# Kernel optimization log

Hardware: AMD Instinct MI355X
Metric: run time of the kernel (lower is better)

## Reference

```python
import jax, jax.numpy as jnp
import numpy as np

B, L, D_IN = 4, 2048, 1024
D_KEY, D_VAL = 1024, 1024
N_SLOTS, TOPK = 32768, 16
TEMP = 0.1
EPS = 1e-5


def layer_norm(x, g, b):
    mu = jnp.mean(x, axis=-1, keepdims=True)
    var = jnp.var(x, axis=-1, keepdims=True)
    return (x - mu) * jax.lax.rsqrt(var + EPS) * g + b


def setup_inputs() -> dict:
    key = jax.random.key(0)
    ks = jax.random.split(key, 8)
    s_in = 1.0 / np.sqrt(D_IN)
    s_ft = 1.0 / np.sqrt(D_IN + D_VAL + 1)
    return {
        "h_in": jax.random.normal(ks[0], (B, L, D_IN), jnp.float32),
        "Wk": jax.random.normal(ks[1], (D_IN, D_KEY), jnp.float32) * s_in,
        "bk": jnp.zeros((D_KEY,), jnp.float32),
        "cube_keys": jax.random.normal(ks[2], (N_SLOTS, D_KEY), jnp.float32),
        "cube_vals": jax.random.normal(ks[3], (N_SLOTS, D_VAL), jnp.float32) * 0.1,
        "ln_in_g": jnp.ones((D_IN,), jnp.float32),
        "ln_in_b": jnp.zeros((D_IN,), jnp.float32),
        "ln_pred_g": jnp.ones((D_VAL,), jnp.float32),
        "ln_pred_b": jnp.zeros((D_VAL,), jnp.float32),
        "W1": jax.random.normal(ks[4], (D_IN + D_VAL + 1, D_IN), jnp.float32) * s_ft,
        "b1": jnp.zeros((D_IN,), jnp.float32),
        "W2": jax.random.normal(ks[5], (D_IN, 1), jnp.float32) * s_in,
        "b2": jnp.zeros((1,), jnp.float32),
    }


def reference(h_in, Wk, bk, cube_keys, cube_vals, ln_in_g, ln_in_b,
              ln_pred_g, ln_pred_b, W1, b1, W2, b2):
    Bv, Lv, Dv = h_in.shape
    # key projection -> [B*L, d_key]
    keys = (jnp.einsum('bld,dk->blk', h_in, Wk) + bk).reshape(Bv * Lv, -1)
    # cube kNN query: cosine similarity against slot keys
    kn = keys * jax.lax.rsqrt(jnp.sum(keys * keys, -1, keepdims=True) + 1e-8)
    mn = cube_keys * jax.lax.rsqrt(jnp.sum(cube_keys * cube_keys, -1, keepdims=True) + 1e-8)
    sims = kn @ mn.T                                   # [BL, N]
    top_sims, idx = jax.lax.top_k(sims, TOPK)          # [BL, K]
    w = jax.nn.softmax(top_sims / TEMP, axis=-1)       # retrieval weights
    vals = jnp.take(cube_vals, idx, axis=0)            # [BL, K, d_val] gather
    pred = jnp.einsum('nk,nkd->nd', w, vals).reshape(Bv, Lv, -1)
    conf = ((top_sims[:, 0] + 1.0) * 0.5).reshape(Bv, Lv, 1)
    # gate
    feats = jnp.concatenate([layer_norm(h_in, ln_in_g, ln_in_b),
                             layer_norm(pred, ln_pred_g, ln_pred_b),
                             conf], axis=-1)
    hmid = jax.nn.silu(jnp.einsum('blf,fd->bld', feats, W1) + b1)
    alpha = jnp.clip(jax.nn.sigmoid(jnp.einsum('bld,do->blo', hmid, W2) + b2), 0.0, 1.0)
    # blend (y_teacher is None): (1-a)*h + a*(h+pred)
    y_out = (1.0 - alpha) * h_in + alpha * (h_in + pred)
    return y_out, jnp.mean(alpha), jnp.mean(conf)
```

## Files before the change

### kernel.cpp

```cpp
#include <hip/hip_runtime.h>
#include <hip/hip_bf16.h>
#include <cstdint>
#include <cstddef>

typedef __bf16 bf16;
typedef __bf16 bf16x4 __attribute__((ext_vector_type(4)));
typedef __bf16 bf16x8 __attribute__((ext_vector_type(8)));
typedef float  f32x4  __attribute__((ext_vector_type(4)));

#define BL      8192
#define DDIM    1024
#define NSLOTS  32768
#define NSPLIT  8
#define SLOTS_PER (NSLOTS / NSPLIT)

#define WS_MN    ((size_t)0)
#define WS_PRED  ((size_t)0)
#define WS_HBF   ((size_t)67108864)
#define WS_HMID  WS_HBF
#define WS_WKT   ((size_t)83886080)
#define WS_W1T   ((size_t)85983232)
#define WS_KEYS  ((size_t)90177536)
#define WS_FEATS WS_KEYS
#define WS_KN    ((size_t)123731968)
#define WS_TPK   ((size_t)140509184)
#define WS_CONF  ((size_t)148897792)

__device__ __forceinline__ void async16(const void* g, void* l) {
  __builtin_amdgcn_global_load_lds(
      (const __attribute__((address_space(1))) void*)g,
      (__attribute__((address_space(3))) void*)(uintptr_t)(uint32_t)(uintptr_t)l,
      16, 0, 0);
}

__device__ __forceinline__ void stage_tile(const bf16* __restrict__ src, int ld,
                                           bf16* lds, int tid) {
  const int wave = tid >> 6;
#pragma unroll
  for (int issue = 0; issue < 2; ++issue) {
    const int gi  = issue * 256 + tid;
    const int row = gi >> 2;
    const int gc  = gi & 3;
    const bf16* g = src + (size_t)row * ld + gc * 8;
    bf16* l = lds + (size_t)(issue * 256 + wave * 64) * 8;
    async16(g, l);
  }
}

__device__ __forceinline__ f32x4 mfma_bf16(bf16x8 a, bf16x8 b, f32x4 c) {
  return __builtin_amdgcn_mfma_f32_16x16x32_bf16(a, b, c, 0, 0, 0);
}

__device__ __forceinline__ float block_sum(float v, float* red) {
#pragma unroll
  for (int off = 32; off > 0; off >>= 1) v += __shfl_xor(v, off, 64);
  const int tid = threadIdx.x;
  if ((tid & 63) == 0) red[tid >> 6] = v;
  __syncthreads();
  v = red[0] + red[1] + red[2] + red[3];
  __syncthreads();
  return v;
}

__global__ void cvt_bf16_kernel(const float* __restrict__ in, bf16* __restrict__ out, int n4) {
  int i = blockIdx.x * blockDim.x + threadIdx.x;
  if (i >= n4) return;
  f32x4 v = *(const f32x4*)(in + (size_t)i * 4);
  bf16x4 o = {(bf16)v.x, (bf16)v.y, (bf16)v.z, (bf16)v.w};
  *(bf16x4*)(out + (size_t)i * 4) = o;
}

__global__ void transpose_f32_bf16(const float* __restrict__ in, bf16* __restrict__ out,
                                   int R, int C) {
  __shared__ float tile[32][33];
  const int c0 = blockIdx.x * 32, r0 = blockIdx.y * 32;
  for (int i = threadIdx.y; i < 32; i += 8)
    tile[i][threadIdx.x] = in[(size_t)(r0 + i) * C + c0 + threadIdx.x];
  __syncthreads();
  for (int i = threadIdx.y; i < 32; i += 8)
    out[(size_t)(c0 + i) * R + r0 + threadIdx.x] = (bf16)tile[threadIdx.x][i];
}

__global__ __launch_bounds__(256) void rownorm_kernel(const float* __restrict__ in,
                                                      bf16* __restrict__ out) {
  __shared__ float red[4];
  const int row = blockIdx.x, t = threadIdx.x;
  f32x4 v = *(const f32x4*)(in + (size_t)row * 1024 + t * 4);
  float sq = v.x * v.x + v.y * v.y + v.z * v.z + v.w * v.w;
  sq = block_sum(sq, red);
  float sc = rsqrtf(sq + 1e-8f);
  bf16x4 o = {(bf16)(v.x * sc), (bf16)(v.y * sc), (bf16)(v.z * sc), (bf16)(v.w * sc)};
  *(bf16x4*)(out + (size_t)row * 1024 + t * 4) = o;
}

template <int EPI>
__global__ __launch_bounds__(256, 2) void gemm_bt_kernel(
    const bf16* __restrict__ A, const bf16* __restrict__ Bm, int Kd,
    float* __restrict__ Cf, bf16* __restrict__ Cb,
    const float* __restrict__ bias, const float* __restrict__ conf,
    const float* __restrict__ w1c) {
  __shared__ bf16 As[128 * 32];
  __shared__ bf16 Bs[128 * 32];
  const int tid = threadIdx.x;
  const int lane = tid & 63, wave = tid >> 6;
  const int wr = (wave >> 1) * 64, wc = (wave & 1) * 64;
  const int m0 = blockIdx.x * 128, n0 = blockIdx.y * 128;
  const int ar = lane & 15, ak = (lane >> 4) * 8;

  f32x4 acc[4][4];
#pragma unroll
  for (int i = 0; i < 4; ++i)
#pragma unroll
    for (int j = 0; j < 4; ++j) acc[i][j] = (f32x4){0.f, 0.f, 0.f, 0.f};

  for (int k0 = 0; k0 < Kd; k0 += 32) {
    __syncthreads();
    stage_tile(A + (size_t)m0 * Kd + k0, Kd, As, tid);
    stage_tile(Bm + (size_t)n0 * Kd + k0, Kd, Bs, tid);
    __syncthreads();
    bf16x8 af[4], bfr[4];
#pragma unroll
    for (int i = 0; i < 4; ++i)
      af[i] = *(const bf16x8*)(As + (wr + i * 16 + ar) * 32 + ak);
#pragma unroll
    for (int j = 0; j < 4; ++j)
      bfr[j] = *(const bf16x8*)(Bs + (wc + j * 16 + ar) * 32 + ak);
#pragma unroll
    for (int i = 0; i < 4; ++i)
#pragma unroll
      for (int j = 0; j < 4; ++j)
        acc[i][j] = mfma_bf16(af[i], bfr[j], acc[i][j]);
  }

  const int mq = (lane >> 4) * 4, nq = lane & 15;
#pragma unroll
  for (int i = 0; i < 4; ++i)
#pragma unroll
    for (int j = 0; j < 4; ++j)
#pragma unroll
      for (int r = 0; r < 4; ++r) {
        const int m = m0 + wr + i * 16 + mq + r;
        const int n = n0 + wc + j * 16 + nq;
        float x = acc[i][j][r];
        if (EPI == 0) {
          Cf[(size_t)m * 1024 + n] = x + bias[n];
        } else {
          x += bias[n] + conf[m] * w1c[n];
          x = x / (1.f + expf(-x));
          Cb[(size_t)m * 1024 + n] = (bf16)x;
        }
      }
}


__device__ __forceinline__ void scan64(const float* __restrict__ cs_row, int base_slot,
                                       uint32_t (&tk)[16], float& thrF) {
#pragma unroll
  for (int g = 0; g < 16; ++g) {
    f32x4 v4 = *(const f32x4*)(cs_row + g * 4);
#pragma unroll
    for (int e = 0; e < 4; ++e) {
      const float v = v4[e];
      if (v > thrF) {
        const uint32_t u = __float_as_uint(v);
        uint32_t cur = ((u ^ 0x80000000u) & 0xFFFF8000u) | (uint32_t)(base_slot + g * 4 + e);
#pragma unroll
        for (int p = 0; p < 16; ++p) {
          const uint32_t old = tk[p];
          const uint32_t mx = old > cur ? old : cur;
          const uint32_t mn_ = old > cur ? cur : old;
          tk[p] = mx;
          cur = mn_;
        }
        thrF = __uint_as_float((tk[15] & 0xFFFF8000u) ^ 0x80000000u);
      }
    }
  }
}

__global__ __launch_bounds__(256, 2) void sims_topk_kernel(
    const bf16* __restrict__ kn, const bf16* __restrict__ mn,
    uint32_t* __restrict__ tpk) {
  __shared__ bf16 As[128 * 32];
  __shared__ bf16 Bs0[128 * 32];
  __shared__ bf16 Bs1[128 * 32];
  __shared__ float Cs[64 * 132];

  const int tid = threadIdx.x;
  const int lane = tid & 63, wave = tid >> 6;
  const int wr = (wave >> 1) * 64, wc = (wave & 1) * 64;
  const int split = blockIdx.x;
  const int m0 = blockIdx.y * 128;
  const int sbeg = split * SLOTS_PER;
  const int ar = lane & 15, ak = (lane >> 4) * 8;
  const int mq = (lane >> 4) * 4, nq = lane & 15;

  const int rowloc = tid & 63;
  const int half = tid >> 7;
  const bool scanA = ((tid & 127) < 64);

  uint32_t tk[16];
#pragma unroll
  for (int j = 0; j < 16; ++j) tk[j] = 0u;
  float thrF = __uint_as_float(0x80000000u);

  for (int it = 0; it < SLOTS_PER / 256; ++it) {
    f32x4 acc[2][4][4];
#pragma unroll
    for (int c = 0; c < 2; ++c)
#pragma unroll
      for (int i = 0; i < 4; ++i)
#pragma unroll
        for (int j = 0; j < 4; ++j) acc[c][i][j] = (f32x4){0.f, 0.f, 0.f, 0.f};

    const int n0 = sbeg + it * 256;
    for (int k0 = 0; k0 < 1024; k0 += 32) {
      __syncthreads();
      stage_tile(kn + (size_t)m0 * 1024 + k0, 1024, As, tid);
      stage_tile(mn + (size_t)n0 * 1024 + k0, 1024, Bs0, tid);
      stage_tile(mn + (size_t)(n0 + 128) * 1024 + k0, 1024, Bs1, tid);
      __syncthreads();
      bf16x8 af[4], b0[4], b1[4];
#pragma unroll
      for (int i = 0; i < 4; ++i)
        af[i] = *(const bf16x8*)(As + (wr + i * 16 + ar) * 32 + ak);
#pragma unroll
      for (int j = 0; j < 4; ++j) {
        b0[j] = *(const bf16x8*)(Bs0 + (wc + j * 16 + ar) * 32 + ak);
        b1[j] = *(const bf16x8*)(Bs1 + (wc + j * 16 + ar) * 32 + ak);
      }
#pragma unroll
      for (int i = 0; i < 4; ++i)
#pragma unroll
        for (int j = 0; j < 4; ++j) {
          acc[0][i][j] = mfma_bf16(af[i], b0[j], acc[0][i][j]);
          acc[1][i][j] = mfma_bf16(af[i], b1[j], acc[1][i][j]);
        }
    }

#pragma unroll
    for (int cc = 0; cc < 2; ++cc) {
      const int slot_base = n0 + cc * 128 + half * 64;
      __syncthreads();
      if (wave < 2) {
#pragma unroll
        for (int i = 0; i < 4; ++i)
#pragma unroll
          for (int j = 0; j < 4; ++j)
#pragma unroll
            for (int r = 0; r < 4; ++r)
              Cs[(i * 16 + mq + r) * 132 + wc + j * 16 + nq] = acc[cc][i][j][r];
      }
      __syncthreads();
      if (scanA) scan64(&Cs[rowloc * 132 + half * 64], slot_base, tk, thrF);
      __syncthreads();
      if (wave >= 2) {
#pragma unroll
        for (int i = 0; i < 4; ++i)
#pragma unroll
          for (int j = 0; j < 4; ++j)
#pragma unroll
            for (int r = 0; r < 4; ++r)
              Cs[(i * 16 + mq + r) * 132 + wc + j * 16 + nq] = acc[cc][i][j][r];
      }
      __syncthreads();
      if (!scanA) scan64(&Cs[rowloc * 132 + half * 64], slot_base, tk, thrF);
    }
  }

  const int row = m0 + (tid & 127);
  uint32_t* dst = tpk + (((size_t)row * NSPLIT + split) * 2 + half) * 16;
#pragma unroll
  for (int j = 0; j < 16; ++j) dst[j] = tk[j];
}

__global__ __launch_bounds__(256) void merge_pred_kernel(
    const uint32_t* __restrict__ tpk, const float* __restrict__ vals,
    float* __restrict__ pred, float* __restrict__ conf) {
  __shared__ uint32_t ks[256];
  __shared__ float sv[16];
  __shared__ int si[16];
  __shared__ float sw[16];
  const int row = blockIdx.x, t = threadIdx.x;
  const uint32_t k = tpk[(size_t)row * 256 + t];
  ks[t] = k;
  __syncthreads();
  int rank = 0;
  for (int j = 0; j < 256; ++j) rank += (ks[j] > k);
  if (rank < 16) {
    sv[rank] = __uint_as_float((k & 0xFFFF8000u) ^ 0x80000000u);
    si[rank] = (int)(k & 0x7FFFu);
  }
  __syncthreads();
  if (t == 0) {
    const float m = sv[0];
    float s = 0.f;
#pragma unroll
    for (int q = 0; q < 16; ++q) {
      float e = expf((sv[q] - m) * 10.f);
      sw[q] = e;
      s += e;
    }
    const float inv = 1.f / s;
#pragma unroll
    for (int q = 0; q < 16; ++q) sw[q] *= inv;
    conf[row] = (m + 1.f) * 0.5f;
  }
  __syncthreads();
  const int col = t * 4;
  f32x4 a = (f32x4){0.f, 0.f, 0.f, 0.f};
#pragma unroll
  for (int q = 0; q < 16; ++q) {
    f32x4 vv = *(const f32x4*)(vals + (size_t)si[q] * 1024 + col);
    a += vv * sw[q];
  }
  *(f32x4*)(pred + (size_t)row * 1024 + col) = a;
}

__global__ __launch_bounds__(256) void feats_kernel(
    const float* __restrict__ h, const float* __restrict__ pred,
    const float* __restrict__ gin, const float* __restrict__ bin,
    const float* __restrict__ gpr, const float* __restrict__ bpr,
    bf16* __restrict__ feats) {
  __shared__ float red[4];
  const int row = blockIdx.x, t = threadIdx.x;
  {
    f32x4 v = *(const f32x4*)(h + (size_t)row * 1024 + t * 4);
    float s = v.x + v.y + v.z + v.w;
    float sq = v.x * v.x + v.y * v.y + v.z * v.z + v.w * v.w;
    s = block_sum(s, red);
    sq = block_sum(sq, red);
    const float mean = s * (1.f / 1024.f);
    const float rstd = rsqrtf(sq * (1.f / 1024.f) - mean * mean + 1e-5f);
    f32x4 g = *(const f32x4*)(gin + t * 4);
    f32x4 b = *(const f32x4*)(bin + t * 4);
    bf16x4 o = {(bf16)((v.x - mean) * rstd * g.x + b.x),
                (bf16)((v.y - mean) * rstd * g.y + b.y),
                (bf16)((v.z - mean) * rstd * g.z + b.z),
                (bf16)((v.w - mean) * rstd * g.w + b.w)};
    *(bf16x4*)(feats + (size_t)row * 2048 + t * 4) = o;
  }
  {
    f32x4 v = *(const f32x4*)(pred + (size_t)row * 1024 + t * 4);
    float s = v.x + v.y + v.z + v.w;
    float sq = v.x * v.x + v.y * v.y + v.z * v.z + v.w * v.w;
    s = block_sum(s, red);
    sq = block_sum(sq, red);
    const float mean = s * (1.f / 1024.f);
    const float rstd = rsqrtf(sq * (1.f / 1024.f) - mean * mean + 1e-5f);
    f32x4 g = *(const f32x4*)(gpr + t * 4);
    f32x4 b = *(const f32x4*)(bpr + t * 4);
    bf16x4 o = {(bf16)((v.x - mean) * rstd * g.x + b.x),
                (bf16)((v.y - mean) * rstd * g.y + b.y),
                (bf16)((v.z - mean) * rstd * g.z + b.z),
                (bf16)((v.w - mean) * rstd * g.w + b.w)};
    *(bf16x4*)(feats + (size_t)row * 2048 + 1024 + t * 4) = o;
  }
}

__global__ __launch_bounds__(256) void final_kernel(
    const bf16* __restrict__ hmid, const float* __restrict__ W2,
    const float* __restrict__ b2, const float* __restrict__ h,
    const float* __restrict__ pred, const float* __restrict__ conf,
    float* __restrict__ out) {
  __shared__ float red[4];
  const int row = blockIdx.x, t = threadIdx.x;
  float s = 0.f;
#pragma unroll
  for (int j = 0; j < 4; ++j) {
    const int c = t + 256 * j;
    s += (float)hmid[(size_t)row * 1024 + c] * W2[c];
  }
  s = block_sum(s, red);
  float alpha = 1.f / (1.f + expf(-(s + b2[0])));
  alpha = fminf(fmaxf(alpha, 0.f), 1.f);
  f32x4 hv = *(const f32x4*)(h + (size_t)row * 1024 + t * 4);
  f32x4 pv = *(const f32x4*)(pred + (size_t)row * 1024 + t * 4);
  f32x4 y = hv + pv * alpha;
  *(f32x4*)(out + (size_t)row * 1024 + t * 4) = y;
  if (t == 0) {
    atomicAdd(out + 8388608, alpha * (1.f / 8192.f));
    atomicAdd(out + 8388609, conf[row] * (1.f / 8192.f));
  }
}

extern "C" void kernel_launch(void* const* d_in, const int* in_sizes, int n_in,
                              void* d_out, int out_size, void* d_ws, size_t ws_size,
                              hipStream_t stream) {
  const float* h_in      = (const float*)d_in[0];
  const float* Wk        = (const float*)d_in[1];
  const float* bk        = (const float*)d_in[2];
  const float* cube_keys = (const float*)d_in[3];
  const float* cube_vals = (const float*)d_in[4];
  const float* ln_in_g   = (const float*)d_in[5];
  const float* ln_in_b   = (const float*)d_in[6];
  const float* ln_pred_g = (const float*)d_in[7];
  const float* ln_pred_b = (const float*)d_in[8];
  const float* W1        = (const float*)d_in[9];
  const float* b1        = (const float*)d_in[10];
  const float* W2        = (const float*)d_in[11];
  const float* b2        = (const float*)d_in[12];

  char* ws = (char*)d_ws;
  bf16*     mn    = (bf16*)(ws + WS_MN);
  float*    pred  = (float*)(ws + WS_PRED);
  bf16*     h_bf  = (bf16*)(ws + WS_HBF);
  bf16*     hmid  = (bf16*)(ws + WS_HMID);
  bf16*     wkT   = (bf16*)(ws + WS_WKT);
  bf16*     w1T   = (bf16*)(ws + WS_W1T);
  float*    keys  = (float*)(ws + WS_KEYS);
  bf16*     feats = (bf16*)(ws + WS_FEATS);
  bf16*     kn    = (bf16*)(ws + WS_KN);
  uint32_t* tpk   = (uint32_t*)(ws + WS_TPK);
  float*    conf  = (float*)(ws + WS_CONF);
  float*    out   = (float*)d_out;
  const float* w1c = W1 + (size_t)2048 * 1024;

  cvt_bf16_kernel<<<(BL * DDIM / 4 + 255) / 256, 256, 0, stream>>>(h_in, h_bf, BL * DDIM / 4);
  transpose_f32_bf16<<<dim3(32, 32), dim3(32, 8), 0, stream>>>(Wk, wkT, 1024, 1024);
  transpose_f32_bf16<<<dim3(32, 64), dim3(32, 8), 0, stream>>>(W1, w1T, 2048, 1024);
  rownorm_kernel<<<NSLOTS, 256, 0, stream>>>(cube_keys, mn);

  gemm_bt_kernel<0><<<dim3(64, 8), 256, 0, stream>>>(h_bf, wkT, 1024, keys, nullptr,
                                                     bk, nullptr, nullptr);
  rownorm_kernel<<<BL, 256, 0, stream>>>(keys, kn);

  sims_topk_kernel<<<dim3(NSPLIT, 64), 256, 0, stream>>>(kn, mn, tpk);

  merge_pred_kernel<<<BL, 256, 0, stream>>>(tpk, cube_vals, pred, conf);

  feats_kernel<<<BL, 256, 0, stream>>>(h_in, pred, ln_in_g, ln_in_b,
                                       ln_pred_g, ln_pred_b, feats);
  gemm_bt_kernel<1><<<dim3(64, 8), 256, 0, stream>>>(feats, w1T, 2048, nullptr, hmid,
                                                     b1, conf, w1c);

  hipMemsetAsync(out + 8388608, 0, 8, stream);
  final_kernel<<<BL, 256, 0, stream>>>(hmid, W2, b2, h_in, pred, conf, out);
}
```

Baseline: 1.628 ms.

## Replace shared-memory score tile scan with per-wave candidate queues and warp drain merge

```diff
diff --git a/kernel.cpp b/kernel.cpp
--- a/kernel.cpp
+++ b/kernel.cpp
@@ -13,6 +13,7 @@
 #define NSLOTS  32768
 #define NSPLIT  8
 #define SLOTS_PER (NSLOTS / NSPLIT)
+#define CAP     49
 
 #define WS_MN    ((size_t)0)
 #define WS_PRED  ((size_t)0)
@@ -60,6 +61,30 @@
   v = red[0] + red[1] + red[2] + red[3];
   __syncthreads();
   return v;
+}
+
+__device__ __forceinline__ uint32_t pack_key(float v, int slot) {
+  return ((__float_as_uint(v) ^ 0x80000000u) & 0xFFFF8000u) | (uint32_t)slot;
+}
+
+__device__ __forceinline__ void drain_merge(uint32_t* cand, int* cnt, int rb_own,
+                                            uint32_t (&tk)[16], float& thrF) {
+  int n = cnt[rb_own];
+  n = n > CAP ? CAP : n;
+  for (int t = 0;; ++t) {
+    if (!__any(t < n)) break;
+    uint32_t cur = 0u;
+    if (t < n) cur = cand[rb_own * CAP + t];
+#pragma unroll
+    for (int p = 0; p < 16; ++p) {
+      const uint32_t old = tk[p];
+      const uint32_t mx = old > cur ? old : cur;
+      tk[p] = mx;
+      cur = old > cur ? cur : old;
+    }
+  }
+  cnt[rb_own] = 0;
+  thrF = __uint_as_float((tk[15] & 0xFFFF8000u) ^ 0x80000000u);
 }
 
 __global__ void cvt_bf16_kernel(const float* __restrict__ in, bf16* __restrict__ out, int n4) {
@@ -152,52 +177,27 @@
       }
 }
 
-
-__device__ __forceinline__ void scan64(const float* __restrict__ cs_row, int base_slot,
-                                       uint32_t (&tk)[16], float& thrF) {
-#pragma unroll
-  for (int g = 0; g < 16; ++g) {
-    f32x4 v4 = *(const f32x4*)(cs_row + g * 4);
-#pragma unroll
-    for (int e = 0; e < 4; ++e) {
-      const float v = v4[e];
-      if (v > thrF) {
-        const uint32_t u = __float_as_uint(v);
-        uint32_t cur = ((u ^ 0x80000000u) & 0xFFFF8000u) | (uint32_t)(base_slot + g * 4 + e);
-#pragma unroll
-        for (int p = 0; p < 16; ++p) {
-          const uint32_t old = tk[p];
-          const uint32_t mx = old > cur ? old : cur;
-          const uint32_t mn_ = old > cur ? cur : old;
-          tk[p] = mx;
-          cur = mn_;
-        }
-        thrF = __uint_as_float((tk[15] & 0xFFFF8000u) ^ 0x80000000u);
-      }
-    }
-  }
-}
-
 __global__ __launch_bounds__(256, 2) void sims_topk_kernel(
     const bf16* __restrict__ kn, const bf16* __restrict__ mn,
     uint32_t* __restrict__ tpk) {
   __shared__ bf16 As[128 * 32];
   __shared__ bf16 Bs0[128 * 32];
   __shared__ bf16 Bs1[128 * 32];
-  __shared__ float Cs[64 * 132];
+  __shared__ uint32_t cand[256 * CAP];
+  __shared__ int cnt[256];
 
   const int tid = threadIdx.x;
   const int lane = tid & 63, wave = tid >> 6;
-  const int wr = (wave >> 1) * 64, wc = (wave & 1) * 64;
+  const int wr = (wave >> 1) * 64;
+  const int ch = wave & 1;
   const int split = blockIdx.x;
   const int m0 = blockIdx.y * 128;
   const int sbeg = split * SLOTS_PER;
   const int ar = lane & 15, ak = (lane >> 4) * 8;
   const int mq = (lane >> 4) * 4, nq = lane & 15;
-
-  const int rowloc = tid & 63;
-  const int half = tid >> 7;
-  const bool scanA = ((tid & 127) < 64);
+  const int rb_own = (wr + lane) * 2 + ch;
+
+  cnt[tid] = 0;
 
   uint32_t tk[16];
 #pragma unroll
@@ -226,8 +226,8 @@
         af[i] = *(const bf16x8*)(As + (wr + i * 16 + ar) * 32 + ak);
 #pragma unroll
       for (int j = 0; j < 4; ++j) {
-        b0[j] = *(const bf16x8*)(Bs0 + (wc + j * 16 + ar) * 32 + ak);
-        b1[j] = *(const bf16x8*)(Bs1 + (wc + j * 16 + ar) * 32 + ak);
+        b0[j] = *(const bf16x8*)(Bs0 + (ch * 64 + j * 16 + ar) * 32 + ak);
+        b1[j] = *(const bf16x8*)(Bs1 + (ch * 64 + j * 16 + ar) * 32 + ak);
       }
 #pragma unroll
       for (int i = 0; i < 4; ++i)
@@ -240,36 +240,52 @@
 
 #pragma unroll
     for (int cc = 0; cc < 2; ++cc) {
-      const int slot_base = n0 + cc * 128 + half * 64;
-      __syncthreads();
-      if (wave < 2) {
+      const int colbase = sbeg + it * 256 + cc * 128 + ch * 64;
+      uint64_t skip = 0ull;
+#pragma unroll
+      for (int i = 0; i < 4; ++i)
+#pragma unroll
+        for (int r = 0; r < 4; ++r) {
+          const int owner = i * 16 + mq + r;
+          const float thr = __shfl(thrF, owner, 64);
+          const int rb = (wr + owner) * 2 + ch;
+#pragma unroll
+          for (int j = 0; j < 4; ++j) {
+            const float v = acc[cc][i][j][r];
+            if (v > thr) {
+              const int old = atomicAdd(&cnt[rb], 1);
+              if (old < CAP) cand[rb * CAP + old] = pack_key(v, colbase + j * 16 + nq);
+              else skip |= (1ull << (i * 16 + r * 4 + j));
+            }
+          }
+        }
+      drain_merge(cand, cnt, rb_own, tk, thrF);
+      if (__any(skip != 0ull)) {
 #pragma unroll
         for (int i = 0; i < 4; ++i)
 #pragma unroll
-          for (int j = 0; j < 4; ++j)
-#pragma unroll
-            for (int r = 0; r < 4; ++r)
-              Cs[(i * 16 + mq + r) * 132 + wc + j * 16 + nq] = acc[cc][i][j][r];
+          for (int r = 0; r < 4; ++r) {
+            const int owner = i * 16 + mq + r;
+            const float thr = __shfl(thrF, owner, 64);
+            const int rb = (wr + owner) * 2 + ch;
+#pragma unroll
+            for (int j = 0; j < 4; ++j) {
+              if (skip & (1ull << (i * 16 + r * 4 + j))) {
+                const float v = acc[cc][i][j][r];
+                if (v > thr) {
+                  const int old = atomicAdd(&cnt[rb], 1);
+                  if (old < CAP) cand[rb * CAP + old] = pack_key(v, colbase + j * 16 + nq);
+                }
+              }
+            }
+          }
+        drain_merge(cand, cnt, rb_own, tk, thrF);
       }
-      __syncthreads();
-      if (scanA) scan64(&Cs[rowloc * 132 + half * 64], slot_base, tk, thrF);
-      __syncthreads();
-      if (wave >= 2) {
-#pragma unroll
-        for (int i = 0; i < 4; ++i)
-#pragma unroll
-          for (int j = 0; j < 4; ++j)
-#pragma unroll
-            for (int r = 0; r < 4; ++r)
-              Cs[(i * 16 + mq + r) * 132 + wc + j * 16 + nq] = acc[cc][i][j][r];
-      }
-      __syncthreads();
-      if (!scanA) scan64(&Cs[rowloc * 132 + half * 64], slot_base, tk, thrF);
     }
   }
 
-  const int row = m0 + (tid & 127);
-  uint32_t* dst = tpk + (((size_t)row * NSPLIT + split) * 2 + half) * 16;
+  const int row = m0 + wr + lane;
+  uint32_t* dst = tpk + (((size_t)row * NSPLIT + split) * 2 + ch) * 16;
 #pragma unroll
   for (int j = 0; j < 16; ++j) dst[j] = tk[j];
 }
```

Result: faster. 1.447 ms (-11.1%).
